# Kernel optimization log

Hardware: AMD Instinct MI355X
Metric: run time of the kernel (lower is better)

## Reference

```python
import jax, jax.numpy as jnp
import numpy as np

def setup_inputs() -> dict:
    key = jax.random.key(0)
    k1, k2, k3 = jax.random.split(key, 3)
    shape = (2, 2048, 8, 64)  # [n, l, h, d]
    return {
        "q": jax.random.normal(k1, shape, dtype=jnp.float32),
        "k": jax.random.normal(k2, shape, dtype=jnp.float32),
        "v": jax.random.normal(k3, shape, dtype=jnp.float32),
    }

def reference(q, k, v):
    # QK^T: [n, l, s, h]
    qk = jnp.einsum('nlhd,nshd->nlsh', q, k)
    softmax_temp = 1.0 / (q.shape[3] ** 0.5)
    attn = jax.nn.softmax(softmax_temp * qk, axis=2)
    # weighted values: [n, l, h, d]
    return jnp.einsum('nlsh,nshd->nlhd', attn, v)
```

## Files before the change

### kernel.cpp

```cpp
#include <hip/hip_runtime.h>
#include <hip/hip_bf16.h>
#include <math.h>

typedef float floatx16 __attribute__((ext_vector_type(16)));
typedef __bf16 bf16x8 __attribute__((ext_vector_type(8)));

#define SEQ 2048
#define NH 8
#define DH 64
#define HEADS 16
#define RS (NH * DH)

__device__ __forceinline__ unsigned int pk2bf(float a, float b) {
  union { __hip_bfloat162 h2; unsigned int u; } c;
  c.h2 = __float22bfloat162_rn(make_float2(a, b));
  return c.u;
}

__device__ __forceinline__ void hswap_fwd(unsigned& a, unsigned& b) {
  asm volatile("v_permlane32_swap_b32 %0, %1" : "+v"(a), "+v"(b));
}
__device__ __forceinline__ void hswap_rev(unsigned& a, unsigned& b) {
  asm volatile("v_permlane32_swap_b32 %0, %1" : "+v"(b), "+v"(a));
}

#define SMEM_BYTES 37376

__global__ __launch_bounds__(512)
void attn(const float* __restrict__ q, const float* __restrict__ k,
          const float* __restrict__ v, float* __restrict__ out) {
  __shared__ __align__(16) char smem[SMEM_BYTES];
  float* oM = (float*)smem;
  float* lM = (float*)(smem + 8 * 16 * 72 * 4);

  const int tid  = threadIdx.x;
  const int wave = tid >> 6;
  const int lane = tid & 63;
  const int l32  = lane & 31;
  const int hl   = lane >> 5;
  const int wq   = wave >> 2;
  const int wk   = wave & 3;

  unsigned px = (unsigned)lane, py = (unsigned)lane + 100u;
  hswap_fwd(px, py);
  const bool mir = (__builtin_amdgcn_readfirstlane(px) != 0u);

  const int bx   = blockIdx.x;
  const int head = bx & 15;
  const int qh2  = bx >> 4;
  const int n = head >> 3, h = head & 7;

  const float* kf = k + ((size_t)n * SEQ * NH + h) * DH;
  const float* vf = v + ((size_t)n * SEQ * NH + h) * DH;

  bf16x8 qB[2][4];
  #pragma unroll
  for (int qs = 0; qs < 2; ++qs)
    #pragma unroll
    for (int kk = 0; kk < 4; ++kk) {
      const int row = qh2 * 128 + wq * 64 + qs * 32 + l32;
      const float* src = q + ((size_t)((n * SEQ + row) * NH + h)) * DH + kk * 16 + hl * 8;
      float4 x0 = *(const float4*)src;
      float4 x1 = *(const float4*)(src + 4);
      union { unsigned int u32[4]; bf16x8 v8; } u;
      u.u32[0] = pk2bf(x0.x, x0.y); u.u32[1] = pk2bf(x0.z, x0.w);
      u.u32[2] = pk2bf(x1.x, x1.y); u.u32[3] = pk2bf(x1.z, x1.w);
      qB[qs][kk] = u.v8;
    }

  floatx16 o[2][2];
  float lsum[2];
  #pragma unroll
  for (int qs = 0; qs < 2; ++qs) {
    lsum[qs] = 0.f;
    #pragma unroll
    for (int d = 0; d < 2; ++d)
      #pragma unroll
      for (int i = 0; i < 16; ++i) o[qs][d][i] = 0.f;
  }

  const float S = 0.125f * 1.4426950408889634f;
  const float C = 12.0f;

  for (int it = 0; it < 8; ++it) {
    const int kt = wk * 8 + it;
    const float* kt_base = kf + (size_t)kt * 64 * RS;
    const float* vt_base = vf + (size_t)kt * 64 * RS;

    bf16x8 kA[2][4];
    #pragma unroll
    for (int ks2 = 0; ks2 < 2; ++ks2)
      #pragma unroll
      for (int kk = 0; kk < 4; ++kk) {
        const float* src = kt_base + (size_t)(ks2 * 32 + l32) * RS + kk * 16 + hl * 8;
        float4 x0 = *(const float4*)src;
        float4 x1 = *(const float4*)(src + 4);
        union { unsigned int u32[4]; bf16x8 v8; } u;
        u.u32[0] = pk2bf(x0.x, x0.y); u.u32[1] = pk2bf(x0.z, x0.w);
        u.u32[2] = pk2bf(x1.x, x1.y); u.u32[3] = pk2bf(x1.z, x1.w);
        kA[ks2][kk] = u.v8;
      }
    bf16x8 vB[4][2];
    #pragma unroll
    for (int ss = 0; ss < 4; ++ss)
      #pragma unroll
      for (int dsub = 0; dsub < 2; ++dsub) {
        const float* src = vt_base + (size_t)(ss * 16 + hl * 8) * RS + dsub * 32 + l32;
        float w0 = src[0 * RS], w1 = src[1 * RS], w2 = src[2 * RS], w3 = src[3 * RS];
        float w4 = src[4 * RS], w5 = src[5 * RS], w6 = src[6 * RS], w7 = src[7 * RS];
        union { unsigned int u32[4]; bf16x8 v8; } u;
        u.u32[0] = pk2bf(w0, w1); u.u32[1] = pk2bf(w2, w3);
        u.u32[2] = pk2bf(w4, w5); u.u32[3] = pk2bf(w6, w7);
        vB[ss][dsub] = u.v8;
      }

    #pragma unroll
    for (int ks2 = 0; ks2 < 2; ++ks2) {
      floatx16 acc2[2];
      #pragma unroll
      for (int i = 0; i < 16; ++i) acc2[0][i] = 0.f;
      #pragma unroll
      for (int kk = 0; kk < 4; ++kk)
        acc2[0] = __builtin_amdgcn_mfma_f32_32x32x16_bf16(kA[ks2][kk], qB[0][kk], acc2[0], 0, 0, 0);

      #pragma unroll
      for (int m = 0; m < 2; ++m) {
        unsigned pk[8];
        #pragma unroll
        for (int g2 = 0; g2 < 4; ++g2) {
          float p0 = __builtin_amdgcn_exp2f(acc2[m][4 * g2 + 0] * S - C);
          float p1 = __builtin_amdgcn_exp2f(acc2[m][4 * g2 + 1] * S - C);
          float p2 = __builtin_amdgcn_exp2f(acc2[m][4 * g2 + 2] * S - C);
          float p3 = __builtin_amdgcn_exp2f(acc2[m][4 * g2 + 3] * S - C);
          lsum[m] += (p0 + p1) + (p2 + p3);
          pk[g2 * 2]     = pk2bf(p0, p1);
          pk[g2 * 2 + 1] = pk2bf(p2, p3);
        }

        if (m == 0) {
          #pragma unroll
          for (int i = 0; i < 16; ++i) acc2[1][i] = 0.f;
          #pragma unroll
          for (int kk = 0; kk < 4; ++kk)
            acc2[1] = __builtin_amdgcn_mfma_f32_32x32x16_bf16(kA[ks2][kk], qB[1][kk], acc2[1], 0, 0, 0);
        }

        union { unsigned u32[4]; bf16x8 v8; } A1, A2;
        A1.u32[0] = pk[0]; A1.u32[2] = pk[2];
        A1.u32[1] = pk[1]; A1.u32[3] = pk[3];
        A2.u32[0] = pk[4]; A2.u32[2] = pk[6];
        A2.u32[1] = pk[5]; A2.u32[3] = pk[7];
        if (!mir) {
          hswap_fwd(A1.u32[0], A1.u32[2]); hswap_fwd(A1.u32[1], A1.u32[3]);
          hswap_fwd(A2.u32[0], A2.u32[2]); hswap_fwd(A2.u32[1], A2.u32[3]);
        } else {
          hswap_rev(A1.u32[0], A1.u32[2]); hswap_rev(A1.u32[1], A1.u32[3]);
          hswap_rev(A2.u32[0], A2.u32[2]); hswap_rev(A2.u32[1], A2.u32[3]);
        }

        o[m][0] = __builtin_amdgcn_mfma_f32_32x32x16_bf16(A1.v8, vB[ks2 * 2][0],     o[m][0], 0, 0, 0);
        o[m][1] = __builtin_amdgcn_mfma_f32_32x32x16_bf16(A1.v8, vB[ks2 * 2][1],     o[m][1], 0, 0, 0);
        o[m][0] = __builtin_amdgcn_mfma_f32_32x32x16_bf16(A2.v8, vB[ks2 * 2 + 1][0], o[m][0], 0, 0, 0);
        o[m][1] = __builtin_amdgcn_mfma_f32_32x32x16_bf16(A2.v8, vB[ks2 * 2 + 1][1], o[m][1], 0, 0, 0);
      }
    }
  }

  #pragma unroll
  for (int qs = 0; qs < 2; ++qs)
    lsum[qs] += __shfl_xor(lsum[qs], 32, 64);

  const int r32  = tid >> 4;
  const int wqr  = r32 >> 4;
  const int prow = r32 & 15;
  const int col4 = tid & 15;
  #pragma unroll
  for (int p = 0; p < 4; ++p) {
    const int qsub = p >> 1, rh = p & 1;
    __syncthreads();
    #pragma unroll
    for (int r8 = 0; r8 < 8; ++r8) {
      const int r   = rh * 8 + r8;
      const int rip = (r8 & 3) + 4 * hl + 8 * (r8 >> 2);
      oM[(wave * 16 + rip) * 72 + l32]      = o[qsub][0][r];
      oM[(wave * 16 + rip) * 72 + 32 + l32] = o[qsub][1][r];
    }
    if (lane < 32 && ((lane >> 4) & 1) == rh) lM[wave * 16 + (lane & 15)] = lsum[qsub];
    __syncthreads();
    float4 s = make_float4(0.f, 0.f, 0.f, 0.f);
    float l = 0.f;
    #pragma unroll
    for (int j = 0; j < 4; ++j) {
      const int w = wqr * 4 + j;
      float4 t4 = *(const float4*)&oM[(w * 16 + prow) * 72 + col4 * 4];
      s.x += t4.x; s.y += t4.y; s.z += t4.z; s.w += t4.w;
      l += lM[w * 16 + prow];
    }
    float inv = 1.f / l;
    const int grow = qh2 * 128 + wqr * 64 + p * 16 + prow;
    float4 st; st.x = s.x * inv; st.y = s.y * inv; st.z = s.z * inv; st.w = s.w * inv;
    *(float4*)(out + ((size_t)((n * SEQ + grow) * NH + h)) * DH + col4 * 4) = st;
  }
}

extern "C" void kernel_launch(void* const* d_in, const int* in_sizes, int n_in,
                              void* d_out, int out_size, void* d_ws, size_t ws_size,
                              hipStream_t stream) {
  const float* q = (const float*)d_in[0];
  const float* k = (const float*)d_in[1];
  const float* v = (const float*)d_in[2];
  float* out = (float*)d_out;
  (void)in_sizes; (void)n_in; (void)out_size; (void)d_ws; (void)ws_size;

  attn<<<HEADS * (SEQ / 128), 512, 0, stream>>>(q, k, v, out);
}
```

Before: 116.5 us.

## Double-buffer V register tiles and prefetch next iteration with scalar base addressing

Prefetches the next iteration's V tile into a second register buffer while the current tile is computed, and fully unrolls the key loop. The per-wave K/V base pointer is made wave-uniform via readfirstlane and per-lane offsets are precomputed. This is meant to hide global-load latency of the strided V gathers behind MFMA and exp work, and to simplify address arithmetic. The trade is higher register pressure, which launch_bounds(512,2) constrains and which may cause spills.

```diff
diff --git a/kernel.cpp b/kernel.cpp
--- a/kernel.cpp
+++ b/kernel.cpp
@@ -26,7 +26,7 @@
 
 #define SMEM_BYTES 37376
 
-__global__ __launch_bounds__(512)
+__global__ __launch_bounds__(512, 2)
 void attn(const float* __restrict__ q, const float* __restrict__ k,
           const float* __restrict__ v, float* __restrict__ out) {
   __shared__ __align__(16) char smem[SMEM_BYTES];
@@ -52,6 +52,12 @@
 
   const float* kf = k + ((size_t)n * SEQ * NH + h) * DH;
   const float* vf = v + ((size_t)n * SEQ * NH + h) * DH;
+
+  const int swk = __builtin_amdgcn_readfirstlane(wk);
+  const float* kq = kf + (size_t)swk * 8 * 64 * RS;
+  const float* vq = vf + (size_t)swk * 8 * 64 * RS;
+  const int klane = l32 * RS + hl * 8;
+  const int vlane = hl * 8 * RS + l32;
 
   bf16x8 qB[2][4];
   #pragma unroll
@@ -79,39 +85,44 @@
       for (int i = 0; i < 16; ++i) o[qs][d][i] = 0.f;
   }
 
+  auto loadV = [&](bf16x8 (&dst)[4][2], int itv) {
+    #pragma unroll
+    for (int ss = 0; ss < 4; ++ss)
+      #pragma unroll
+      for (int dsub = 0; dsub < 2; ++dsub) {
+        const float* src = vq + itv * 64 * RS + ss * 16 * RS + vlane + dsub * 32;
+        float w0 = src[0 * RS], w1 = src[1 * RS], w2 = src[2 * RS], w3 = src[3 * RS];
+        float w4 = src[4 * RS], w5 = src[5 * RS], w6 = src[6 * RS], w7 = src[7 * RS];
+        union { unsigned int u32[4]; bf16x8 v8; } u;
+        u.u32[0] = pk2bf(w0, w1); u.u32[1] = pk2bf(w2, w3);
+        u.u32[2] = pk2bf(w4, w5); u.u32[3] = pk2bf(w6, w7);
+        dst[ss][dsub] = u.v8;
+      }
+  };
+
+  bf16x8 vB[2][4][2];
+  loadV(vB[0], 0);
+
   const float S = 0.125f * 1.4426950408889634f;
   const float C = 12.0f;
 
+  #pragma unroll
   for (int it = 0; it < 8; ++it) {
-    const int kt = wk * 8 + it;
-    const float* kt_base = kf + (size_t)kt * 64 * RS;
-    const float* vt_base = vf + (size_t)kt * 64 * RS;
+    const int cb = it & 1;
+    if (it < 7) loadV(vB[cb ^ 1], it + 1);
 
     bf16x8 kA[2][4];
     #pragma unroll
     for (int ks2 = 0; ks2 < 2; ++ks2)
       #pragma unroll
       for (int kk = 0; kk < 4; ++kk) {
-        const float* src = kt_base + (size_t)(ks2 * 32 + l32) * RS + kk * 16 + hl * 8;
+        const float* src = kq + it * 64 * RS + ks2 * 32 * RS + klane + kk * 16;
         float4 x0 = *(const float4*)src;
         float4 x1 = *(const float4*)(src + 4);
         union { unsigned int u32[4]; bf16x8 v8; } u;
         u.u32[0] = pk2bf(x0.x, x0.y); u.u32[1] = pk2bf(x0.z, x0.w);
         u.u32[2] = pk2bf(x1.x, x1.y); u.u32[3] = pk2bf(x1.z, x1.w);
         kA[ks2][kk] = u.v8;
-      }
-    bf16x8 vB[4][2];
-    #pragma unroll
-    for (int ss = 0; ss < 4; ++ss)
-      #pragma unroll
-      for (int dsub = 0; dsub < 2; ++dsub) {
-        const float* src = vt_base + (size_t)(ss * 16 + hl * 8) * RS + dsub * 32 + l32;
-        float w0 = src[0 * RS], w1 = src[1 * RS], w2 = src[2 * RS], w3 = src[3 * RS];
-        float w4 = src[4 * RS], w5 = src[5 * RS], w6 = src[6 * RS], w7 = src[7 * RS];
-        union { unsigned int u32[4]; bf16x8 v8; } u;
-        u.u32[0] = pk2bf(w0, w1); u.u32[1] = pk2bf(w2, w3);
-        u.u32[2] = pk2bf(w4, w5); u.u32[3] = pk2bf(w6, w7);
-        vB[ss][dsub] = u.v8;
       }
 
     #pragma unroll
@@ -158,10 +169,10 @@
           hswap_rev(A2.u32[0], A2.u32[2]); hswap_rev(A2.u32[1], A2.u32[3]);
         }
 
-        o[m][0] = __builtin_amdgcn_mfma_f32_32x32x16_bf16(A1.v8, vB[ks2 * 2][0],     o[m][0], 0, 0, 0);
-        o[m][1] = __builtin_amdgcn_mfma_f32_32x32x16_bf16(A1.v8, vB[ks2 * 2][1],     o[m][1], 0, 0, 0);
-        o[m][0] = __builtin_amdgcn_mfma_f32_32x32x16_bf16(A2.v8, vB[ks2 * 2 + 1][0], o[m][0], 0, 0, 0);
-        o[m][1] = __builtin_amdgcn_mfma_f32_32x32x16_bf16(A2.v8, vB[ks2 * 2 + 1][1], o[m][1], 0, 0, 0);
+        o[m][0] = __builtin_amdgcn_mfma_f32_32x32x16_bf16(A1.v8, vB[cb][ks2 * 2][0],     o[m][0], 0, 0, 0);
+        o[m][1] = __builtin_amdgcn_mfma_f32_32x32x16_bf16(A1.v8, vB[cb][ks2 * 2][1],     o[m][1], 0, 0, 0);
+        o[m][0] = __builtin_amdgcn_mfma_f32_32x32x16_bf16(A2.v8, vB[cb][ks2 * 2 + 1][0], o[m][0], 0, 0, 0);
+        o[m][1] = __builtin_amdgcn_mfma_f32_32x32x16_bf16(A2.v8, vB[cb][ks2 * 2 + 1][1], o[m][1], 0, 0, 0);
       }
     }
   }
```

Result: slower. 342.2 us (+193.8%).
